# Kernel tuning notes

Measured on AMD Instinct MI355X. Metric: run time of the kernel, lower is better.

## Reference

```python
import jax, jax.numpy as jnp
import numpy as np

N_NODES = 100_000
N_EDGES = 1_600_000
N_GRAPHS = 32
D_IN = 64
D_H1 = 64
D_H2 = 64
D_OUT = 10


def setup_inputs() -> dict:
    key = jax.random.key(0)
    ks = jax.random.split(key, 6)
    x = jax.random.normal(ks[0], (N_NODES, D_IN), dtype=jnp.float32)
    edge_index = jax.random.randint(ks[1], (2, N_EDGES), 0, N_NODES, dtype=jnp.int32)
    edge_weight = jax.random.uniform(ks[2], (N_EDGES,), dtype=jnp.float32)
    # deterministic sorted graph assignment: every one of the 32 graphs nonempty
    batch = ((jnp.arange(N_NODES) * N_GRAPHS) // N_NODES).astype(jnp.int32)
    W1 = jax.random.normal(ks[3], (D_IN, D_H1), dtype=jnp.float32) * 0.1
    b1 = jnp.zeros((D_H1,), dtype=jnp.float32)
    W2 = jax.random.normal(ks[4], (D_H1, D_H2), dtype=jnp.float32) * 0.1
    b2 = jnp.zeros((D_H2,), dtype=jnp.float32)
    Wlin = jax.random.normal(ks[5], (D_H2, D_OUT), dtype=jnp.float32) * 0.1
    blin = jnp.zeros((D_OUT,), dtype=jnp.float32)
    return {"x": x, "edge_index": edge_index, "edge_weight": edge_weight,
            "batch": batch, "W1": W1, "b1": b1, "W2": W2, "b2": b2,
            "Wlin": Wlin, "blin": blin}


def _gcn_norm(edge_index, edge_weight, n_nodes):
    """GCNConv(improved=True) normalization: add self-loops with weight 2.0,
    then norm_e = deg(dst)^-1/2 * w_e * deg(src)^-1/2."""
    loop = jnp.arange(n_nodes, dtype=edge_index.dtype)
    src = jnp.concatenate([edge_index[0], loop])
    dst = jnp.concatenate([edge_index[1], loop])
    w = jnp.concatenate([edge_weight, jnp.full((n_nodes,), 2.0, edge_weight.dtype)])
    deg = jax.ops.segment_sum(w, dst, num_segments=n_nodes)
    dinv = jnp.where(deg > 0, jax.lax.rsqrt(deg), 0.0)
    norm = dinv[src] * w * dinv[dst]
    return src, dst, norm


def _gcn_conv(h, W, b, src, dst, norm, n_nodes):
    hw = h @ W                                   # [N, d_out] transform first
    msg = hw[src] * norm[:, None]                # gather + scale  [E+N, d_out]
    return jax.ops.segment_sum(msg, dst, num_segments=n_nodes) + b


def reference(x, edge_index, edge_weight, batch, W1, b1, W2, b2, Wlin, blin):
    n = x.shape[0]
    src, dst, norm = _gcn_norm(edge_index, edge_weight, n)
    h = jax.nn.relu(_gcn_conv(x, W1, b1, src, dst, norm, n))
    h = jax.nn.relu(_gcn_conv(h, W2, b2, src, dst, norm, n))
    pooled = jax.ops.segment_max(h, batch, num_segments=N_GRAPHS)  # [G, d_h2]
    return pooled @ Wlin + blin
```

## Files before the change

### kernel.cpp

```cpp
#include <hip/hip_runtime.h>

#define N_NODES 100000
#define N_GRAPHS 32
#define N_EDGES 1600000
#define NODES_PER_GRAPH 3125
#define D 64
#define DOUT 10
#define CAP 64
#define PARTS 8
#define PART_NODES 12500
#define NCHUNK 782
#define CHUNK_EDGES 2048
#define EDGE_BLOCKS (PARTS * NCHUNK)
#define GEMM_BLOCKS 6250
#define WQ 32767.0f
#define POOL_SLICES 16
#define NODE_BLOCKS 25000

typedef float f32x4 __attribute__((ext_vector_type(4)));

__device__ __forceinline__ unsigned short f2bf(float x) {
    unsigned u = __float_as_uint(x);
    u += 0x7FFFu + ((u >> 16) & 1u);
    return (unsigned short)(u >> 16);
}
__device__ __forceinline__ float bf2f(unsigned short h) {
    return __uint_as_float((unsigned)h << 16);
}
__device__ __forceinline__ float bflo(unsigned u) { return __uint_as_float(u << 16); }
__device__ __forceinline__ float bfhi(unsigned u) { return __uint_as_float(u & 0xFFFF0000u); }

__global__ void k_init(int* cnt, unsigned int* pooled) {
    int i = blockIdx.x * blockDim.x + threadIdx.x;
    if (i < N_NODES) cnt[i] = 0;
    if (i < N_GRAPHS * D) pooled[i] = 0u;
}

__global__ void k_fill_gemm(const int* __restrict__ src, const int* __restrict__ dst,
                            const float* __restrict__ w, int* cnt,
                            unsigned int* __restrict__ bucket,
                            const float* __restrict__ X, const float* __restrict__ W,
                            unsigned short* __restrict__ Y) {
    __shared__ float4 Ws[64 * 16];
    if (blockIdx.x < EDGE_BLOCKS) {
        int p = blockIdx.x & 7;
        int chunk = blockIdx.x >> 3;
        int base = chunk * CHUNK_EDGES;
        int lo = p * PART_NODES, hi = lo + PART_NODES;
#pragma unroll
        for (int j = 0; j < 8; ++j) {
            int e = base + j * 256 + threadIdx.x;
            if (e < N_EDGES) {
                int d = __builtin_nontemporal_load(&dst[e]);
                if (d >= lo && d < hi) {
                    int pos = atomicAdd(&cnt[d], 1);
                    if (pos < CAP) {
                        float wv = __builtin_nontemporal_load(&w[e]);
                        int sv = __builtin_nontemporal_load(&src[e]);
                        unsigned int wq = (unsigned int)(wv * WQ + 0.5f);
                        bucket[d * CAP + pos] = ((unsigned int)sv << 15) | wq;
                    }
                }
            }
        }
    } else {
        int t = threadIdx.x;
        const float4* W4 = (const float4*)W;
        for (int i = t; i < 1024; i += 256) Ws[i] = W4[i];
        __syncthreads();
        int row = (blockIdx.x - EDGE_BLOCKS) * 16 + (t >> 4);
        int c4 = t & 15;
        const f32x4* xr4 = (const f32x4*)(X + (size_t)row * D);
        float4 acc = {0.f, 0.f, 0.f, 0.f};
#pragma unroll
        for (int k4 = 0; k4 < 16; ++k4) {
            f32x4 xv = __builtin_nontemporal_load(&xr4[k4]);
            float4 w0 = Ws[(k4 * 4 + 0) * 16 + c4];
            float4 w1 = Ws[(k4 * 4 + 1) * 16 + c4];
            float4 w2 = Ws[(k4 * 4 + 2) * 16 + c4];
            float4 w3 = Ws[(k4 * 4 + 3) * 16 + c4];
            acc.x += xv.x * w0.x + xv.y * w1.x + xv.z * w2.x + xv.w * w3.x;
            acc.y += xv.x * w0.y + xv.y * w1.y + xv.z * w2.y + xv.w * w3.y;
            acc.z += xv.x * w0.z + xv.y * w1.z + xv.z * w2.z + xv.w * w3.z;
            acc.w += xv.x * w0.w + xv.y * w1.w + xv.z * w2.w + xv.w * w3.w;
        }
        ushort4 o;
        o.x = f2bf(acc.x); o.y = f2bf(acc.y); o.z = f2bf(acc.z); o.w = f2bf(acc.w);
        ((ushort4*)Y)[(size_t)row * 16 + c4] = o;
    }
}

__device__ __forceinline__ int swiz_node(int bidx, int tid) {
    return ((bidx & 7) * (NODE_BLOCKS / 8) + (bidx >> 3)) * 4 + (tid >> 6);
}

__global__ void k_deg(const int* __restrict__ cnt, const unsigned int* __restrict__ bucket,
                      float* __restrict__ dinv) {
    int node = swiz_node(blockIdx.x, threadIdx.x);
    int lane = threadIdx.x & 63;
    int c = cnt[node];
    if (c > CAP) c = CAP;
    float wv = 0.0f;
    if (lane < c) wv = (float)(bucket[node * CAP + lane] & 32767u);
#pragma unroll
    for (int off = 1; off < 64; off <<= 1) wv += __shfl_xor(wv, off);
    if (lane == 0) dinv[node] = rsqrtf(2.0f + wv * (1.0f / WQ));
}

__global__ void k_gather8_bf16(const int* __restrict__ cnt, const unsigned int* __restrict__ bucket,
                               const uint4* __restrict__ hw8, const float* __restrict__ dinv,
                               const float* __restrict__ b, uint4* __restrict__ outb) {
    int node = swiz_node(blockIdx.x, threadIdx.x);
    int lane = threadIdx.x & 63;
    int g = lane >> 3, q = lane & 7;
    int end = cnt[node];
    if (end > CAP) end = CAP;
    float dvd = dinv[node];
    float wsc = dvd * (1.0f / WQ);
    const unsigned int* bk = bucket + node * CAP;
    float a0=0.f,a1=0.f,a2=0.f,a3=0.f,a4=0.f,a5=0.f,a6=0.f,a7=0.f;
    if (g == 0) {
        float s = 2.0f * dvd * dvd;
        uint4 u = hw8[(size_t)node * 8 + q];
        a0 = bflo(u.x)*s; a1 = bfhi(u.x)*s; a2 = bflo(u.y)*s; a3 = bfhi(u.y)*s;
        a4 = bflo(u.z)*s; a5 = bfhi(u.z)*s; a6 = bflo(u.w)*s; a7 = bfhi(u.w)*s;
    }
    int e = g;
    for (; e + 8 < end; e += 16) {
        unsigned int e0 = bk[e];
        unsigned int e1 = bk[e + 8];
        int s0 = e0 >> 15, s1 = e1 >> 15;
        float d0 = dinv[s0], d1 = dinv[s1];
        uint4 u0 = hw8[(size_t)s0 * 8 + q];
        uint4 u1 = hw8[(size_t)s1 * 8 + q];
        float n0 = d0 * (float)(e0 & 32767u) * wsc;
        float n1 = d1 * (float)(e1 & 32767u) * wsc;
        a0 += bflo(u0.x)*n0 + bflo(u1.x)*n1; a1 += bfhi(u0.x)*n0 + bfhi(u1.x)*n1;
        a2 += bflo(u0.y)*n0 + bflo(u1.y)*n1; a3 += bfhi(u0.y)*n0 + bfhi(u1.y)*n1;
        a4 += bflo(u0.z)*n0 + bflo(u1.z)*n1; a5 += bfhi(u0.z)*n0 + bfhi(u1.z)*n1;
        a6 += bflo(u0.w)*n0 + bflo(u1.w)*n1; a7 += bfhi(u0.w)*n0 + bfhi(u1.w)*n1;
    }
    for (; e < end; e += 8) {
        unsigned int ee = bk[e];
        int s = ee >> 15;
        float nrm = dinv[s] * (float)(ee & 32767u) * wsc;
        uint4 u = hw8[(size_t)s * 8 + q];
        a0 += bflo(u.x)*nrm; a1 += bfhi(u.x)*nrm;
        a2 += bflo(u.y)*nrm; a3 += bfhi(u.y)*nrm;
        a4 += bflo(u.z)*nrm; a5 += bfhi(u.z)*nrm;
        a6 += bflo(u.w)*nrm; a7 += bfhi(u.w)*nrm;
    }
    a0 += __shfl_xor(a0, 8);  a1 += __shfl_xor(a1, 8);
    a2 += __shfl_xor(a2, 8);  a3 += __shfl_xor(a3, 8);
    a4 += __shfl_xor(a4, 8);  a5 += __shfl_xor(a5, 8);
    a6 += __shfl_xor(a6, 8);  a7 += __shfl_xor(a7, 8);
    a0 += __shfl_xor(a0, 16); a1 += __shfl_xor(a1, 16);
    a2 += __shfl_xor(a2, 16); a3 += __shfl_xor(a3, 16);
    a4 += __shfl_xor(a4, 16); a5 += __shfl_xor(a5, 16);
    a6 += __shfl_xor(a6, 16); a7 += __shfl_xor(a7, 16);
    a0 += __shfl_xor(a0, 32); a1 += __shfl_xor(a1, 32);
    a2 += __shfl_xor(a2, 32); a3 += __shfl_xor(a3, 32);
    a4 += __shfl_xor(a4, 32); a5 += __shfl_xor(a5, 32);
    a6 += __shfl_xor(a6, 32); a7 += __shfl_xor(a7, 32);
    if (g == 0) {
        float4 b0 = ((const float4*)b)[2 * q];
        float4 b1 = ((const float4*)b)[2 * q + 1];
        uint4 r;
        r.x = (unsigned)f2bf(fmaxf(a0 + b0.x, 0.f)) | ((unsigned)f2bf(fmaxf(a1 + b0.y, 0.f)) << 16);
        r.y = (unsigned)f2bf(fmaxf(a2 + b0.z, 0.f)) | ((unsigned)f2bf(fmaxf(a3 + b0.w, 0.f)) << 16);
        r.z = (unsigned)f2bf(fmaxf(a4 + b1.x, 0.f)) | ((unsigned)f2bf(fmaxf(a5 + b1.y, 0.f)) << 16);
        r.w = (unsigned)f2bf(fmaxf(a6 + b1.z, 0.f)) | ((unsigned)f2bf(fmaxf(a7 + b1.w, 0.f)) << 16);
        outb[(size_t)node * 8 + q] = r;
    }
}

__global__ void k_gemm64b(const unsigned short* __restrict__ Xb, const float* __restrict__ W,
                          unsigned short* __restrict__ Y) {
    __shared__ float4 Ws[64 * 16];
    int t = threadIdx.x;
    const float4* W4 = (const float4*)W;
    for (int i = t; i < 1024; i += 256) Ws[i] = W4[i];
    __syncthreads();
    int row = blockIdx.x * 16 + (t >> 4);
    int c4 = t & 15;
    const uint4* xr = (const uint4*)(Xb + (size_t)row * D);
    uint4 u8[8];
#pragma unroll
    for (int m = 0; m < 8; ++m) u8[m] = xr[m];
    float4 acc = {0.f, 0.f, 0.f, 0.f};
#pragma unroll
    for (int k4 = 0; k4 < 16; ++k4) {
        uint4 uu = u8[k4 >> 1];
        unsigned ua = (k4 & 1) ? uu.z : uu.x;
        unsigned ub = (k4 & 1) ? uu.w : uu.y;
        float xv0 = bflo(ua), xv1 = bfhi(ua), xv2 = bflo(ub), xv3 = bfhi(ub);
        float4 w0 = Ws[(k4 * 4 + 0) * 16 + c4];
        float4 w1 = Ws[(k4 * 4 + 1) * 16 + c4];
        float4 w2 = Ws[(k4 * 4 + 2) * 16 + c4];
        float4 w3 = Ws[(k4 * 4 + 3) * 16 + c4];
        acc.x += xv0 * w0.x + xv1 * w1.x + xv2 * w2.x + xv3 * w3.x;
        acc.y += xv0 * w0.y + xv1 * w1.y + xv2 * w2.y + xv3 * w3.y;
        acc.z += xv0 * w0.z + xv1 * w1.z + xv2 * w2.z + xv3 * w3.z;
        acc.w += xv0 * w0.w + xv1 * w1.w + xv2 * w2.w + xv3 * w3.w;
    }
    ushort4 o;
    o.x = f2bf(acc.x); o.y = f2bf(acc.y); o.z = f2bf(acc.z); o.w = f2bf(acc.w);
    ((ushort4*)Y)[(size_t)row * 16 + c4] = o;
}

__global__ void k_pool(const unsigned short* __restrict__ h, unsigned int* pooled) {
    __shared__ float2 s[256];
    int g = blockIdx.x / POOL_SLICES;
    int slice = blockIdx.x % POOL_SLICES;
    int t = threadIdx.x;
    int f2 = t & 31;
    int r = t >> 5;
    float m0 = 0.0f, m1 = 0.0f;
    const unsigned int* hu = (const unsigned int*)(h + (size_t)g * NODES_PER_GRAPH * D);
    for (int i = slice * 8 + r; i < NODES_PER_GRAPH; i += 8 * POOL_SLICES) {
        unsigned int u = hu[(size_t)i * 32 + f2];
        m0 = fmaxf(m0, bflo(u));
        m1 = fmaxf(m1, bfhi(u));
    }
    s[t].x = m0; s[t].y = m1;
    __syncthreads();
    if (t < 128) { s[t].x = fmaxf(s[t].x, s[t + 128].x); s[t].y = fmaxf(s[t].y, s[t + 128].y); }
    __syncthreads();
    if (t < 64)  { s[t].x = fmaxf(s[t].x, s[t + 64].x);  s[t].y = fmaxf(s[t].y, s[t + 64].y); }
    __syncthreads();
    if (t < 32) {
        atomicMax(&pooled[g * D + 2 * t],     __float_as_uint(fmaxf(s[t].x, s[t + 32].x)));
        atomicMax(&pooled[g * D + 2 * t + 1], __float_as_uint(fmaxf(s[t].y, s[t + 32].y)));
    }
}

__global__ void k_final(const float* __restrict__ pooled, const float* __restrict__ Wlin,
                        const float* __restrict__ blin, float* __restrict__ out) {
    int t = threadIdx.x;
    if (t < N_GRAPHS * DOUT) {
        int g = t / DOUT, o = t % DOUT;
        float acc = blin[o];
#pragma unroll
        for (int f = 0; f < D; ++f) acc += pooled[g * D + f] * Wlin[f * DOUT + o];
        out[t] = acc;
    }
}

extern "C" void kernel_launch(void* const* d_in, const int* in_sizes, int n_in,
                              void* d_out, int out_size, void* d_ws, size_t ws_size,
                              hipStream_t stream) {
    const float* x     = (const float*)d_in[0];
    const int*   ei    = (const int*)d_in[1];
    const int*   src   = ei;
    const int*   dst   = ei + N_EDGES;
    const float* ew    = (const float*)d_in[2];
    const float* W1    = (const float*)d_in[4];
    const float* b1    = (const float*)d_in[5];
    const float* W2    = (const float*)d_in[6];
    const float* b2    = (const float*)d_in[7];
    const float* Wlin  = (const float*)d_in[8];
    const float* blin  = (const float*)d_in[9];
    float* out = (float*)d_out;

    unsigned int* bucket = (unsigned int*)d_ws;
    unsigned short* hwA = (unsigned short*)(bucket + (size_t)N_NODES * CAP);
    unsigned short* h1b = hwA + (size_t)N_NODES * D;
    unsigned short* hwB = h1b + (size_t)N_NODES * D;
    unsigned short* h2  = hwB + (size_t)N_NODES * D;
    float* dinv   = (float*)(h2 + (size_t)N_NODES * D);
    float* pooled = dinv + N_NODES;
    int*   cnt    = (int*)(pooled + N_GRAPHS * D);

    const int B = 256;
    int gN = (N_NODES + B - 1) / B;

    k_init<<<gN, B, 0, stream>>>(cnt, (unsigned int*)pooled);
    k_fill_gemm<<<EDGE_BLOCKS + GEMM_BLOCKS, B, 0, stream>>>(src, dst, ew, cnt, bucket, x, W1, hwA);
    k_deg<<<NODE_BLOCKS, B, 0, stream>>>(cnt, bucket, dinv);

    k_gather8_bf16<<<NODE_BLOCKS, B, 0, stream>>>(cnt, bucket, (const uint4*)hwA, dinv, b1, (uint4*)h1b);
    k_gemm64b<<<GEMM_BLOCKS, B, 0, stream>>>(h1b, W2, hwB);
    k_gather8_bf16<<<NODE_BLOCKS, B, 0, stream>>>(cnt, bucket, (const uint4*)hwB, dinv, b2, (uint4*)h2);

    k_pool<<<N_GRAPHS * POOL_SLICES, B, 0, stream>>>(h2, (unsigned int*)pooled);
    k_final<<<1, 320, 0, stream>>>(pooled, Wlin, blin, out);
}
```

Measured before the change: 322.8 us.

## Accumulate quantized degree via atomics in fill and drop separate degree kernel

Adds an atomicAdd of the quantized edge weight into a per-node integer degree during bucket filling, removing the k_deg kernel that re-read all buckets. Gather kernels now compute the inverse square-root degree on the fly from the integer degree for each source and destination node. This saves one kernel launch and a full pass over the bucket array. In exchange it adds 1.6M extra atomics in the fill stage and extra rsqrt work per edge in both gather passes. It also changes semantics slightly, since edges beyond CAP are still not counted, same as before.

```diff
diff --git a/kernel.cpp b/kernel.cpp
--- a/kernel.cpp
+++ b/kernel.cpp
@@ -30,14 +30,18 @@
 __device__ __forceinline__ float bflo(unsigned u) { return __uint_as_float(u << 16); }
 __device__ __forceinline__ float bfhi(unsigned u) { return __uint_as_float(u & 0xFFFF0000u); }
 
-__global__ void k_init(int* cnt, unsigned int* pooled) {
+__device__ __forceinline__ float dinv_of(int dq) {
+    return rsqrtf(2.0f + (float)dq * (1.0f / WQ));
+}
+
+__global__ void k_init(int* cnt, int* degq, unsigned int* pooled) {
     int i = blockIdx.x * blockDim.x + threadIdx.x;
-    if (i < N_NODES) cnt[i] = 0;
+    if (i < N_NODES) { cnt[i] = 0; degq[i] = 0; }
     if (i < N_GRAPHS * D) pooled[i] = 0u;
 }
 
 __global__ void k_fill_gemm(const int* __restrict__ src, const int* __restrict__ dst,
-                            const float* __restrict__ w, int* cnt,
+                            const float* __restrict__ w, int* cnt, int* degq,
                             unsigned int* __restrict__ bucket,
                             const float* __restrict__ X, const float* __restrict__ W,
                             unsigned short* __restrict__ Y) {
@@ -58,6 +62,7 @@
                         float wv = __builtin_nontemporal_load(&w[e]);
                         int sv = __builtin_nontemporal_load(&src[e]);
                         unsigned int wq = (unsigned int)(wv * WQ + 0.5f);
+                        atomicAdd(&degq[d], (int)wq);
                         bucket[d * CAP + pos] = ((unsigned int)sv << 15) | wq;
                     }
                 }
@@ -94,28 +99,15 @@
     return ((bidx & 7) * (NODE_BLOCKS / 8) + (bidx >> 3)) * 4 + (tid >> 6);
 }
 
-__global__ void k_deg(const int* __restrict__ cnt, const unsigned int* __restrict__ bucket,
-                      float* __restrict__ dinv) {
-    int node = swiz_node(blockIdx.x, threadIdx.x);
-    int lane = threadIdx.x & 63;
-    int c = cnt[node];
-    if (c > CAP) c = CAP;
-    float wv = 0.0f;
-    if (lane < c) wv = (float)(bucket[node * CAP + lane] & 32767u);
-#pragma unroll
-    for (int off = 1; off < 64; off <<= 1) wv += __shfl_xor(wv, off);
-    if (lane == 0) dinv[node] = rsqrtf(2.0f + wv * (1.0f / WQ));
-}
-
 __global__ void k_gather8_bf16(const int* __restrict__ cnt, const unsigned int* __restrict__ bucket,
-                               const uint4* __restrict__ hw8, const float* __restrict__ dinv,
+                               const uint4* __restrict__ hw8, const int* __restrict__ degq,
                                const float* __restrict__ b, uint4* __restrict__ outb) {
     int node = swiz_node(blockIdx.x, threadIdx.x);
     int lane = threadIdx.x & 63;
     int g = lane >> 3, q = lane & 7;
     int end = cnt[node];
     if (end > CAP) end = CAP;
-    float dvd = dinv[node];
+    float dvd = dinv_of(degq[node]);
     float wsc = dvd * (1.0f / WQ);
     const unsigned int* bk = bucket + node * CAP;
     float a0=0.f,a1=0.f,a2=0.f,a3=0.f,a4=0.f,a5=0.f,a6=0.f,a7=0.f;
@@ -130,7 +122,7 @@
         unsigned int e0 = bk[e];
         unsigned int e1 = bk[e + 8];
         int s0 = e0 >> 15, s1 = e1 >> 15;
-        float d0 = dinv[s0], d1 = dinv[s1];
+        float d0 = dinv_of(degq[s0]), d1 = dinv_of(degq[s1]);
         uint4 u0 = hw8[(size_t)s0 * 8 + q];
         uint4 u1 = hw8[(size_t)s1 * 8 + q];
         float n0 = d0 * (float)(e0 & 32767u) * wsc;
@@ -143,7 +135,7 @@
     for (; e < end; e += 8) {
         unsigned int ee = bk[e];
         int s = ee >> 15;
-        float nrm = dinv[s] * (float)(ee & 32767u) * wsc;
+        float nrm = dinv_of(degq[s]) * (float)(ee & 32767u) * wsc;
         uint4 u = hw8[(size_t)s * 8 + q];
         a0 += bflo(u.x)*nrm; a1 += bfhi(u.x)*nrm;
         a2 += bflo(u.y)*nrm; a3 += bfhi(u.y)*nrm;
@@ -267,20 +259,19 @@
     unsigned short* h1b = hwA + (size_t)N_NODES * D;
     unsigned short* hwB = h1b + (size_t)N_NODES * D;
     unsigned short* h2  = hwB + (size_t)N_NODES * D;
-    float* dinv   = (float*)(h2 + (size_t)N_NODES * D);
-    float* pooled = dinv + N_NODES;
+    int*   degq   = (int*)(h2 + (size_t)N_NODES * D);
+    float* pooled = (float*)(degq + N_NODES);
     int*   cnt    = (int*)(pooled + N_GRAPHS * D);
 
     const int B = 256;
     int gN = (N_NODES + B - 1) / B;
 
-    k_init<<<gN, B, 0, stream>>>(cnt, (unsigned int*)pooled);
-    k_fill_gemm<<<EDGE_BLOCKS + GEMM_BLOCKS, B, 0, stream>>>(src, dst, ew, cnt, bucket, x, W1, hwA);
-    k_deg<<<NODE_BLOCKS, B, 0, stream>>>(cnt, bucket, dinv);
-
-    k_gather8_bf16<<<NODE_BLOCKS, B, 0, stream>>>(cnt, bucket, (const uint4*)hwA, dinv, b1, (uint4*)h1b);
+    k_init<<<gN, B, 0, stream>>>(cnt, degq, (unsigned int*)pooled);
+    k_fill_gemm<<<EDGE_BLOCKS + GEMM_BLOCKS, B, 0, stream>>>(src, dst, ew, cnt, degq, bucket, x, W1, hwA);
+
+    k_gather8_bf16<<<NODE_BLOCKS, B, 0, stream>>>(cnt, bucket, (const uint4*)hwA, degq, b1, (uint4*)h1b);
     k_gemm64b<<<GEMM_BLOCKS, B, 0, stream>>>(h1b, W2, hwB);
-    k_gather8_bf16<<<NODE_BLOCKS, B, 0, stream>>>(cnt, bucket, (const uint4*)hwB, dinv, b2, (uint4*)h2);
+    k_gather8_bf16<<<NODE_BLOCKS, B, 0, stream>>>(cnt, bucket, (const uint4*)hwB, degq, b2, (uint4*)h2);
 
     k_pool<<<N_GRAPHS * POOL_SLICES, B, 0, stream>>>(h2, (unsigned int*)pooled);
     k_final<<<1, 320, 0, stream>>>(pooled, Wlin, blin, out);
```

Measured after the change: 373.4 us. +15.7%, slower.
